# Optimization experiments

Measured on AMD Instinct MI355X. Metric: run time of the kernel, lower is better.

The kernel has to match this reference:

```python
import jax, jax.numpy as jnp
import numpy as np

HEADS = 4
TOKEN_CH = 128
D_HEAD = TOKEN_CH // HEADS  # 32


def setup_inputs() -> dict:
    key = jax.random.key(0)
    ks = jax.random.split(key, 12)
    B, QC, Z, H, W = 4, 256, 16, 32, 32
    N, KVC = 256, 512
    s = lambda k, shape, fan: jax.random.normal(k, shape, jnp.float32) * (1.0 / np.sqrt(fan))
    return {
        "feat":   jax.random.normal(ks[0], (B, QC, Z, H, W), jnp.float32),
        "tokens": jax.random.normal(ks[1], (B, N, KVC), jnp.float32),
        "qw":   s(ks[2], (TOKEN_CH, QC), QC),      # Conv3d 1x1 -> [out, in]
        "qb":   jnp.zeros((TOKEN_CH,), jnp.float32),
        "kw":   s(ks[3], (TOKEN_CH, KVC), KVC),    # Linear, no bias
        "vw":   s(ks[4], (TOKEN_CH, KVC), KVC),
        "projw": s(ks[5], (QC, TOKEN_CH), TOKEN_CH),
        "projb": jnp.zeros((QC,), jnp.float32),
        "ff1w": s(ks[6], (QC * 2, QC), QC),
        "ff1b": jnp.zeros((QC * 2,), jnp.float32),
        "ff2w": s(ks[7], (QC, QC * 2), QC * 2),
        "ff2b": jnp.zeros((QC,), jnp.float32),
        "gate": jnp.zeros((1,), jnp.float32),
    }


def _conv1x1(x, w, b):
    # x: [B, Cin, Z, H, W], w: [Cout, Cin] -> [B, Cout, Z, H, W]
    return jnp.einsum('bczhw,oc->bozhw', x, w) + b[None, :, None, None, None]


def reference(feat, tokens, qw, qb, kw, vw, projw, projb, ff1w, ff1b, ff2w, ff2b, gate):
    B, C, Z, H, W = feat.shape
    S = Z * H * W
    scale = D_HEAD ** (-0.5)

    # Q: conv1x1 then split heads -> [B, nh, S, dh]
    q = _conv1x1(feat, qw, qb).reshape(B, HEADS, D_HEAD, S).transpose(0, 1, 3, 2)
    # K, V: linear (no bias) -> [B, nh, N, dh]
    k = jnp.einsum('bnc,tc->bnt', tokens, kw).reshape(B, -1, HEADS, D_HEAD).transpose(0, 2, 1, 3)
    v = jnp.einsum('bnc,tc->bnt', tokens, vw).reshape(B, -1, HEADS, D_HEAD).transpose(0, 2, 1, 3)

    attn = jax.nn.softmax(jnp.einsum('bhsd,bhnd->bhsn', q, k) * scale, axis=-1)
    out = jnp.einsum('bhsn,bhnd->bhsd', attn, v)  # [B, nh, S, dh]

    # merge heads back to channel-first volume: b (nh dh) z h w
    out = out.transpose(0, 1, 3, 2).reshape(B, TOKEN_CH, Z, H, W)
    out = _conv1x1(out, projw, projb)

    out = feat + jnp.tanh(gate[0]) * out
    ff = _conv1x1(jax.nn.silu(_conv1x1(out, ff1w, ff1b)), ff2w, ff2b)
    return out + ff
```

## Files before the change

### kernel.cpp

```cpp
#include <hip/hip_runtime.h>

#define NB 4
#define QC 256
#define SD 16384
#define NT 256
#define KVC 512
#define TC 128
#define NH 4
#define DH 32
#define TSP 64

typedef unsigned short u16;
typedef unsigned int u32;
typedef __attribute__((ext_vector_type(8))) short bf16x8;
typedef __attribute__((ext_vector_type(4))) float f32x4;

__device__ __forceinline__ float b2f(u16 u) {
  unsigned int v = ((unsigned int)u) << 16;
  return __builtin_bit_cast(float, v);
}
__device__ __forceinline__ u16 f2b(float f) {
  unsigned int x = __builtin_bit_cast(unsigned int, f);
  unsigned int r = (x + 0x7fffu + ((x >> 16) & 1u)) >> 16;
  return (u16)r;
}
__device__ __forceinline__ u16 f2b_fast(float f) {
  return (u16)((__builtin_bit_cast(unsigned int, f) + 0x8000u) >> 16);
}
__device__ __forceinline__ u32 pk2(float a, float b) {
  u32 ua = __builtin_bit_cast(u32, a) + 0x8000u;
  u32 ub = __builtin_bit_cast(u32, b) + 0x8000u;
  return __builtin_amdgcn_perm(ub, ua, 0x07060302u);
}

__device__ __forceinline__ int swz(int row, int col) {
  return (row << 8) + (col ^ ((row & 7) << 3));
}
__device__ __forceinline__ int swzH(int row, int col) {
  return (row << 7) + (col ^ ((row & 7) << 3));
}

__global__ __launch_bounds__(256) void prep_kernel(
    const float* __restrict__ ff1w, const float* __restrict__ ff2w,
    u16* __restrict__ w1p, u16* __restrict__ w2p,
    const float* __restrict__ tokens, const float* __restrict__ kw,
    const float* __restrict__ vw, const float* __restrict__ gate,
    float* __restrict__ ws_kv) {
  int bid = blockIdx.x;
  if (bid < 128) {
    int idx = bid * 256 + threadIdx.x;
    int lane = idx & 63;
    int m = lane & 15, q = lane >> 4;
    if (idx < 16384) {
      int kblk = (idx >> 6) & 7;
      int jblk = idx >> 9;
      const float* src = ff1w + (size_t)(jblk * 16 + m) * QC + kblk * 32 + q * 8;
      u16* dst = w1p + (size_t)idx * 8;
#pragma unroll
      for (int i = 0; i < 8; i++) dst[i] = f2b(src[i]);
    } else {
      int s2 = idx - 16384;
      int kblk = (s2 >> 6) & 15;
      int oblk = s2 >> 10;
      const float* src = ff2w + (size_t)(oblk * 16 + m) * KVC + kblk * 32 + q * 8;
      u16* dst = w2p + (size_t)s2 * 8;
#pragma unroll
      for (int i = 0; i < 8; i++) dst[i] = f2b(src[i]);
    }
  }
  float tg = tanhf(gate[0]);
  if (tg == 0.0f) return;
  {
    int b = bid >> 8;
    int n = bid & 255;
    __shared__ float tok[KVC];
    for (int c = threadIdx.x; c < KVC; c += 256)
      tok[c] = tokens[((size_t)(b * NT + n)) * KVC + c];
    __syncthreads();
    int tid = threadIdx.x;
    int t = tid & 127;
    const float* w = (tid < 128) ? kw : vw;
    const float* wr = w + (size_t)t * KVC;
    float acc = 0.f;
    for (int c = 0; c < KVC; c += 4) {
      float4 wv = *(const float4*)(wr + c);
      acc += tok[c] * wv.x + tok[c + 1] * wv.y + tok[c + 2] * wv.z + tok[c + 3] * wv.w;
    }
    int h = t >> 5, d = t & 31;
    float* dst = ws_kv + ((tid < 128) ? 0 : NB * NH * NT * DH);
    dst[(((b * NH + h) * NT) + n) * DH + d] = acc;
  }
}

__global__ __launch_bounds__(512, 4) void fused_kernel(
    const float* __restrict__ feat, const float* __restrict__ qw,
    const float* __restrict__ qb, const float* __restrict__ projw,
    const float* __restrict__ projb, const float* __restrict__ ff1b,
    const float* __restrict__ ff2b, const u16* __restrict__ w1p,
    const u16* __restrict__ w2p, const float* __restrict__ gate,
    const float* __restrict__ ws_kv, float* __restrict__ out) {
  __shared__ u16 sX[64 * 256];
  __shared__ u16 sH[2][64 * 128];

  int b = blockIdx.x >> 8;
  int s0 = (blockIdx.x & 255) * TSP;
  int tid = threadIdx.x;
  int w = tid >> 6;
  int lane = tid & 63;
  int lm = lane & 15, lq = lane >> 4;

  {
    const float* fb = feat + (((size_t)b * QC) << 14) + s0;
    int cq = (tid >> 4) * 4;
    int sq = (tid & 15) * 4;
#pragma unroll
    for (int it = 0; it < 2; ++it) {
      int c = it * 128 + cq;
      float4 r0 = *(const float4*)(fb + ((size_t)(c + 0) << 14) + sq);
      float4 r1 = *(const float4*)(fb + ((size_t)(c + 1) << 14) + sq);
      float4 r2 = *(const float4*)(fb + ((size_t)(c + 2) << 14) + sq);
      float4 r3 = *(const float4*)(fb + ((size_t)(c + 3) << 14) + sq);
      uint2 d0, d1, d2, d3;
      d0.x = pk2(r0.x, r1.x); d0.y = pk2(r2.x, r3.x);
      d1.x = pk2(r0.y, r1.y); d1.y = pk2(r2.y, r3.y);
      d2.x = pk2(r0.z, r1.z); d2.y = pk2(r2.z, r3.z);
      d3.x = pk2(r0.w, r1.w); d3.y = pk2(r2.w, r3.w);
      *(uint2*)&sX[swz(sq + 0, c)] = d0;
      *(uint2*)&sX[swz(sq + 1, c)] = d1;
      *(uint2*)&sX[swz(sq + 2, c)] = d2;
      *(uint2*)&sX[swz(sq + 3, c)] = d3;
    }
  }
  float tg = tanhf(gate[0]);
  __syncthreads();

  if (tg != 0.0f) {
    if (w < 4) {
      float qreg[DH];
#pragma unroll
      for (int d = 0; d < DH; d++) {
        int o = w * DH + d;
        float a = qb[o];
        const float* qr = qw + (size_t)o * QC;
        for (int c = 0; c < QC; c += 4) {
          float4 wv = *(const float4*)(qr + c);
          a += b2f(sX[swz(lane, c + 0)]) * wv.x;
          a += b2f(sX[swz(lane, c + 1)]) * wv.y;
          a += b2f(sX[swz(lane, c + 2)]) * wv.z;
          a += b2f(sX[swz(lane, c + 3)]) * wv.w;
        }
        qreg[d] = a;
      }
      const float* Kp = ws_kv + (size_t)(b * NH + w) * NT * DH;
      const float* Vp = Kp + NB * NH * NT * DH;
      float m_ = -1e30f, l_ = 0.f;
      float oacc[DH];
#pragma unroll
      for (int d = 0; d < DH; d++) oacc[d] = 0.f;
      const float scale = 0.17677669529663687f;
      for (int n = 0; n < NT; n++) {
        const float* kr = Kp + n * DH;
        float s = 0.f;
#pragma unroll
        for (int d = 0; d < DH; d++) s += qreg[d] * kr[d];
        s *= scale;
        float nm = fmaxf(m_, s);
        float p = __expf(s - nm);
        float al = __expf(m_ - nm);
        const float* vr = Vp + n * DH;
        l_ = l_ * al + p;
#pragma unroll
        for (int d = 0; d < DH; d++) oacc[d] = oacc[d] * al + p * vr[d];
        m_ = nm;
      }
      float inv = 1.0f / l_;
#pragma unroll
      for (int d = 0; d < DH; d++)
        sH[0][swzH(lane, w * DH + d)] = f2b(oacc[d] * inv);
    }
    __syncthreads();
    for (int ci = 0; ci < 32; ci++) {
      int c = w * 32 + ci;
      float a = projb[c];
      const float* pr = projw + (size_t)c * TC;
      for (int t = 0; t < TC; t += 4) {
        float4 wv = *(const float4*)(pr + t);
        a += b2f(sH[0][swzH(lane, t + 0)]) * wv.x;
        a += b2f(sH[0][swzH(lane, t + 1)]) * wv.y;
        a += b2f(sH[0][swzH(lane, t + 2)]) * wv.z;
        a += b2f(sH[0][swzH(lane, t + 3)]) * wv.w;
      }
      float o1 = b2f(sX[swz(lane, c)]) + tg * a;
      sX[swz(lane, c)] = f2b(o1);
    }
    __syncthreads();
  }

  f32x4 acc2[2][4];
#pragma unroll
  for (int t = 0; t < 2; t++) {
    float b2v = ff2b[(w * 2 + t) * 16 + lm];
    f32x4 iv = {b2v, b2v, b2v, b2v};
#pragma unroll
    for (int m = 0; m < 4; m++) acc2[t][m] = iv;
  }

#pragma unroll 1
  for (int ch = 0; ch < 4; ++ch) {
    u16* sHh = sH[ch & 1];
    f32x4 acc1[4];
    {
      float b1v = ff1b[(ch * 8 + w) * 16 + lm];
      f32x4 iv = {b1v, b1v, b1v, b1v};
#pragma unroll
      for (int m = 0; m < 4; m++) acc1[m] = iv;
    }
    {
      const u16* p0 = w1p + (((size_t)(ch * 8 + w) * 8) * 64 + lane) * 8;
      bf16x8 c0 = *(const bf16x8*)(p0);
      bf16x8 n0 = *(const bf16x8*)(p0 + 512);
#pragma unroll
      for (int k = 0; k < 8; ++k) {
        bf16x8 f0;
        if (k < 6) f0 = *(const bf16x8*)(p0 + (size_t)(k + 2) * 512);
        int col = k * 32 + lq * 8;
#pragma unroll
        for (int m = 0; m < 4; m++) {
          bf16x8 a = *(const bf16x8*)&sX[swz(m * 16 + lm, col)];
          acc1[m] = __builtin_amdgcn_mfma_f32_16x16x32_bf16(a, c0, acc1[m], 0, 0, 0);
        }
        c0 = n0;
        if (k < 6) n0 = f0;
      }
    }
    {
      int jl = w * 16 + lm;
#pragma unroll
      for (int m = 0; m < 4; m++) {
        int sb = m * 16 + lq * 4;
        f32x4 v = acc1[m];
#pragma unroll
        for (int r = 0; r < 4; r++) {
          float x = v[r];
          float sl = x * __builtin_amdgcn_rcpf(1.f + __expf(-x));
          sHh[swzH(sb + r, jl)] = f2b_fast(sl);
        }
      }
    }
    const u16* qp0 = w2p + (((size_t)((w * 2) * 16 + ch * 4)) * 64 + lane) * 8;
    const u16* qp1 = qp0 + 8192;
    bf16x8 d0 = *(const bf16x8*)(qp0);
    bf16x8 d1 = *(const bf16x8*)(qp1);
    bf16x8 e0 = *(const bf16x8*)(qp0 + 512);
    bf16x8 e1 = *(const bf16x8*)(qp1 + 512);
    __syncthreads();
#pragma unroll
    for (int k = 0; k < 4; ++k) {
      bf16x8 f0, f1;
      if (k < 2) {
        f0 = *(const bf16x8*)(qp0 + (size_t)(k + 2) * 512);
        f1 = *(const bf16x8*)(qp1 + (size_t)(k + 2) * 512);
      }
      int col = k * 32 + lq * 8;
#pragma unroll
      for (int m = 0; m < 4; m++) {
        bf16x8 a = *(const bf16x8*)&sHh[swzH(m * 16 + lm, col)];
        acc2[0][m] = __builtin_amdgcn_mfma_f32_16x16x32_bf16(a, d0, acc2[0][m], 0, 0, 0);
        acc2[1][m] = __builtin_amdgcn_mfma_f32_16x16x32_bf16(a, d1, acc2[1][m], 0, 0, 0);
      }
      d0 = e0; d1 = e1;
      if (k < 2) { e0 = f0; e1 = f1; }
    }
  }

#pragma unroll
  for (int t = 0; t < 2; t++) {
    int c = (w * 2 + t) * 16 + lm;
#pragma unroll
    for (int m = 0; m < 4; m++) {
      int sb = m * 16 + lq * 4;
      f32x4 v = acc2[t][m];
      float4 ov;
      ov.x = v[0] + b2f(sX[swz(sb + 0, c)]);
      ov.y = v[1] + b2f(sX[swz(sb + 1, c)]);
      ov.z = v[2] + b2f(sX[swz(sb + 2, c)]);
      ov.w = v[3] + b2f(sX[swz(sb + 3, c)]);
      *(float4*)(out + (((size_t)(b * QC + c)) << 14) + s0 + sb) = ov;
    }
  }
}

extern "C" void kernel_launch(void* const* d_in, const int* in_sizes, int n_in,
                              void* d_out, int out_size, void* d_ws, size_t ws_size,
                              hipStream_t stream) {
  const float* feat   = (const float*)d_in[0];
  const float* tokens = (const float*)d_in[1];
  const float* qw     = (const float*)d_in[2];
  const float* qb     = (const float*)d_in[3];
  const float* kw     = (const float*)d_in[4];
  const float* vw     = (const float*)d_in[5];
  const float* projw  = (const float*)d_in[6];
  const float* projb  = (const float*)d_in[7];
  const float* ff1w   = (const float*)d_in[8];
  const float* ff1b   = (const float*)d_in[9];
  const float* ff2w   = (const float*)d_in[10];
  const float* ff2b   = (const float*)d_in[11];
  const float* gate   = (const float*)d_in[12];
  float* out = (float*)d_out;

  u16* w1p = (u16*)d_ws;
  u16* w2p = w1p + 131072;
  float* ws_kv = (float*)((char*)d_ws + 524288);

  prep_kernel<<<dim3(NB * NT), dim3(256), 0, stream>>>(
      ff1w, ff2w, w1p, w2p, tokens, kw, vw, gate, ws_kv);
  fused_kernel<<<dim3(NB * (SD / TSP)), dim3(512), 0, stream>>>(
      feat, qw, qb, projw, projb, ff1b, ff2b, w1p, w2p, gate, ws_kv, out);
}
```

Before: 171.4 us.

## Tile FFN GEMMs as 2x2 warp grid and adjust LDS swizzle

Changes the warp decomposition of both FFN MFMA GEMMs from each warp covering all 64 spatial rows to a 2D split (row half by column group), so each warp loads fewer A fragments from LDS per MFMA and reuses them across more weight tiles. The weight prefetch pipeline is reshaped to match, with 2 or 4 B fragments in flight per step. The LDS swizzle now XORs using row>>1 instead of row, which changes the bank-conflict pattern. The extra B fragments and accumulators raise register pressure under the 512-thread, 4-block launch bound.

After: 171.6 us. No clear change (+0.1%).

```diff
diff --git a/kernel.cpp b/kernel.cpp
--- a/kernel.cpp
+++ b/kernel.cpp
@@ -34,10 +34,10 @@
 }
 
 __device__ __forceinline__ int swz(int row, int col) {
-  return (row << 8) + (col ^ ((row & 7) << 3));
+  return (row << 8) + (col ^ (((row >> 1) & 7) << 3));
 }
 __device__ __forceinline__ int swzH(int row, int col) {
-  return (row << 7) + (col ^ ((row & 7) << 3));
+  return (row << 7) + (col ^ (((row >> 1) & 7) << 3));
 }
 
 __global__ __launch_bounds__(256) void prep_kernel(
@@ -108,6 +108,8 @@
   int w = tid >> 6;
   int lane = tid & 63;
   int lm = lane & 15, lq = lane >> 4;
+  int wcol = w >> 1;
+  int wrow = w & 1;
 
   {
     const float* fb = feat + (((size_t)b * QC) << 14) + s0;
@@ -196,49 +198,56 @@
     __syncthreads();
   }
 
-  f32x4 acc2[2][4];
-#pragma unroll
-  for (int t = 0; t < 2; t++) {
-    float b2v = ff2b[(w * 2 + t) * 16 + lm];
+  f32x4 acc2[4][2];
+#pragma unroll
+  for (int t = 0; t < 4; t++) {
+    float b2v = ff2b[(wcol * 4 + t) * 16 + lm];
     f32x4 iv = {b2v, b2v, b2v, b2v};
 #pragma unroll
-    for (int m = 0; m < 4; m++) acc2[t][m] = iv;
+    for (int mi = 0; mi < 2; mi++) acc2[t][mi] = iv;
   }
 
 #pragma unroll 1
   for (int ch = 0; ch < 4; ++ch) {
     u16* sHh = sH[ch & 1];
-    f32x4 acc1[4];
+    f32x4 acc1[2][2];
+#pragma unroll
+    for (int jt = 0; jt < 2; jt++) {
+      float b1v = ff1b[(ch * 8 + wcol * 2 + jt) * 16 + lm];
+      f32x4 iv = {b1v, b1v, b1v, b1v};
+#pragma unroll
+      for (int mi = 0; mi < 2; mi++) acc1[jt][mi] = iv;
+    }
     {
-      float b1v = ff1b[(ch * 8 + w) * 16 + lm];
-      f32x4 iv = {b1v, b1v, b1v, b1v};
-#pragma unroll
-      for (int m = 0; m < 4; m++) acc1[m] = iv;
-    }
-    {
-      const u16* p0 = w1p + (((size_t)(ch * 8 + w) * 8) * 64 + lane) * 8;
+      int jb0 = ch * 8 + wcol * 2;
+      const u16* p0 = w1p + (((size_t)jb0 * 8) * 64 + lane) * 8;
+      const u16* p1 = p0 + 4096;
       bf16x8 c0 = *(const bf16x8*)(p0);
-      bf16x8 n0 = *(const bf16x8*)(p0 + 512);
+      bf16x8 c1 = *(const bf16x8*)(p1);
 #pragma unroll
       for (int k = 0; k < 8; ++k) {
-        bf16x8 f0;
-        if (k < 6) f0 = *(const bf16x8*)(p0 + (size_t)(k + 2) * 512);
+        bf16x8 n0, n1;
+        if (k < 7) {
+          n0 = *(const bf16x8*)(p0 + (size_t)(k + 1) * 512);
+          n1 = *(const bf16x8*)(p1 + (size_t)(k + 1) * 512);
+        }
         int col = k * 32 + lq * 8;
 #pragma unroll
-        for (int m = 0; m < 4; m++) {
-          bf16x8 a = *(const bf16x8*)&sX[swz(m * 16 + lm, col)];
-          acc1[m] = __builtin_amdgcn_mfma_f32_16x16x32_bf16(a, c0, acc1[m], 0, 0, 0);
+        for (int mi = 0; mi < 2; mi++) {
+          bf16x8 a = *(const bf16x8*)&sX[swz((wrow * 2 + mi) * 16 + lm, col)];
+          acc1[0][mi] = __builtin_amdgcn_mfma_f32_16x16x32_bf16(a, c0, acc1[0][mi], 0, 0, 0);
+          acc1[1][mi] = __builtin_amdgcn_mfma_f32_16x16x32_bf16(a, c1, acc1[1][mi], 0, 0, 0);
         }
-        c0 = n0;
-        if (k < 6) n0 = f0;
-      }
-    }
-    {
-      int jl = w * 16 + lm;
-#pragma unroll
-      for (int m = 0; m < 4; m++) {
-        int sb = m * 16 + lq * 4;
-        f32x4 v = acc1[m];
+        if (k < 7) { c0 = n0; c1 = n1; }
+      }
+    }
+#pragma unroll
+    for (int jt = 0; jt < 2; jt++) {
+      int jl = (wcol * 2 + jt) * 16 + lm;
+#pragma unroll
+      for (int mi = 0; mi < 2; mi++) {
+        int sb = (wrow * 2 + mi) * 16 + lq * 4;
+        f32x4 v = acc1[jt][mi];
 #pragma unroll
         for (int r = 0; r < 4; r++) {
           float x = v[r];
@@ -247,39 +256,41 @@
         }
       }
     }
-    const u16* qp0 = w2p + (((size_t)((w * 2) * 16 + ch * 4)) * 64 + lane) * 8;
-    const u16* qp1 = qp0 + 8192;
-    bf16x8 d0 = *(const bf16x8*)(qp0);
-    bf16x8 d1 = *(const bf16x8*)(qp1);
-    bf16x8 e0 = *(const bf16x8*)(qp0 + 512);
-    bf16x8 e1 = *(const bf16x8*)(qp1 + 512);
+    const u16* qp = w2p + (((size_t)(wcol * 4) * 16 + ch * 4) * 64 + lane) * 8;
+    bf16x8 d0 = *(const bf16x8*)(qp);
+    bf16x8 d1 = *(const bf16x8*)(qp + 8192);
+    bf16x8 d2 = *(const bf16x8*)(qp + 16384);
+    bf16x8 d3 = *(const bf16x8*)(qp + 24576);
     __syncthreads();
 #pragma unroll
     for (int k = 0; k < 4; ++k) {
-      bf16x8 f0, f1;
-      if (k < 2) {
-        f0 = *(const bf16x8*)(qp0 + (size_t)(k + 2) * 512);
-        f1 = *(const bf16x8*)(qp1 + (size_t)(k + 2) * 512);
+      bf16x8 e0, e1, e2, e3;
+      if (k < 3) {
+        e0 = *(const bf16x8*)(qp + (size_t)(k + 1) * 512);
+        e1 = *(const bf16x8*)(qp + 8192 + (size_t)(k + 1) * 512);
+        e2 = *(const bf16x8*)(qp + 16384 + (size_t)(k + 1) * 512);
+        e3 = *(const bf16x8*)(qp + 24576 + (size_t)(k + 1) * 512);
       }
       int col = k * 32 + lq * 8;
 #pragma unroll
-      for (int m = 0; m < 4; m++) {
-        bf16x8 a = *(const bf16x8*)&sHh[swzH(m * 16 + lm, col)];
-        acc2[0][m] = __builtin_amdgcn_mfma_f32_16x16x32_bf16(a, d0, acc2[0][m], 0, 0, 0);
-        acc2[1][m] = __builtin_amdgcn_mfma_f32_16x16x32_bf16(a, d1, acc2[1][m], 0, 0, 0);
-      }
-      d0 = e0; d1 = e1;
-      if (k < 2) { e0 = f0; e1 = f1; }
-    }
-  }
-
-#pragma unroll
-  for (int t = 0; t < 2; t++) {
-    int c = (w * 2 + t) * 16 + lm;
-#pragma unroll
-    for (int m = 0; m < 4; m++) {
-      int sb = m * 16 + lq * 4;
-      f32x4 v = acc2[t][m];
+      for (int mi = 0; mi < 2; mi++) {
+        bf16x8 a = *(const bf16x8*)&sHh[swzH((wrow * 2 + mi) * 16 + lm, col)];
+        acc2[0][mi] = __builtin_amdgcn_mfma_f32_16x16x32_bf16(a, d0, acc2[0][mi], 0, 0, 0);
+        acc2[1][mi] = __builtin_amdgcn_mfma_f32_16x16x32_bf16(a, d1, acc2[1][mi], 0, 0, 0);
+        acc2[2][mi] = __builtin_amdgcn_mfma_f32_16x16x32_bf16(a, d2, acc2[2][mi], 0, 0, 0);
+        acc2[3][mi] = __builtin_amdgcn_mfma_f32_16x16x32_bf16(a, d3, acc2[3][mi], 0, 0, 0);
+      }
+      if (k < 3) { d0 = e0; d1 = e1; d2 = e2; d3 = e3; }
+    }
+  }
+
+#pragma unroll
+  for (int t = 0; t < 4; t++) {
+    int c = (wcol * 4 + t) * 16 + lm;
+#pragma unroll
+    for (int mi = 0; mi < 2; mi++) {
+      int sb = (wrow * 2 + mi) * 16 + lq * 4;
+      f32x4 v = acc2[t][mi];
       float4 ov;
       ov.x = v[0] + b2f(sX[swz(sb + 0, c)]);
       ov.y = v[1] + b2f(sX[swz(sb + 1, c)]);
```
